# Kernel optimization log

Hardware: AMD Instinct MI355X
Metric: run time of the kernel (lower is better)

The kernel has to match this reference:

```python
import jax, jax.numpy as jnp
import numpy as np

B, L = 8, 512
D_MODEL, N_HEAD, N_GLOBAL, N_ITER = 64, 8, 64, 4
DAMP_H = 0.0; DAMP_Z = 0.0; STEP_H = 1.0; STEP_Z = 1.0; REG_H = 1.0; REG_Z = 1.0
NEG = -1e9; BIG = 1e9


def sin_pe(length, d):
    # standard additive sinusoidal positional encoding (AddPositionalEncoding)
    pos = np.arange(length, dtype=np.float32)[:, None]
    div = np.exp(np.arange(0, d, 2, dtype=np.float32) * (-np.log(10000.0) / d))
    pe = np.zeros((length, d), dtype=np.float32)
    pe[:, 0::2] = np.sin(pos * div)
    pe[:, 1::2] = np.cos(pos * div)
    return jnp.asarray(pe)


def setup_inputs() -> dict:
    key = jax.random.key(0)
    k1, k2, k3 = jax.random.split(key, 3)
    x = jax.random.normal(k1, (B, L, D_MODEL), jnp.float32)
    mask = jnp.ones((B, L), jnp.int32)
    ternary = jax.random.normal(k2, (D_MODEL, D_MODEL, N_HEAD), jnp.float32)  # std=1 init
    global_w = jax.random.normal(k3, (N_GLOBAL, D_MODEL, 1), jnp.float32) / np.sqrt(D_MODEL)
    return {"x": x, "mask": mask, "ternary": ternary, "global_w": global_w}


def _forward(x, mask, ternary, global_w):
    Bq, Lq, d = x.shape
    norm = lambda a: jax.nn.softmax(a, axis=-1)
    valid = (mask != 0)
    m1 = valid[:, :, None].astype(x.dtype)                      # (B,L,1) keep-mask
    pair = valid[:, None, :, None] & valid[:, None, None, :]    # (B,1,L,L)
    eye_big = BIG * jnp.eye(Lq, dtype=x.dtype)[None, None]      # kill self-edges

    x = x + sin_pe(Lq, d)[None]
    unary = x * m1
    q_z = unary
    q_h1 = jnp.where(pair, 1.0 - eye_big, NEG)                  # (B,H,L,L) via broadcast
    q_h1 = jnp.broadcast_to(q_h1, (Bq, N_HEAD, Lq, Lq))
    q_h2 = jnp.ones((Bq, 1, Lq, N_GLOBAL), x.dtype)             # single-channel: 1 global head

    cache_qh1, cache_qh2 = q_h1, q_h2
    cache_norm_qz = norm(q_z)
    cache_norm_qh1 = norm(q_h1)
    cache_norm_qh2 = norm(q_h2)

    for it in range(N_ITER):
        cache_qz = q_z
        nz = norm(q_z)
        qzn = nz if it == 0 else (1 - STEP_Z) * cache_norm_qz + STEP_Z * nz
        cache_norm_qz = qzn
        qz = qzn * m1
        # F1[z,c,i,j] = sum_{a,b} qz[z,i,a] qz[z,j,b] T[a,b,c]
        t1 = jnp.einsum('zia,abc->zibc', qz, ternary)
        F1 = jnp.einsum('zibc,zjb->zcij', t1, qz)
        F2 = jnp.einsum('zia,jac->zcij', qz, global_w)          # (B,1,L,n_global)
        q_h1 = cache_qh1 * DAMP_H + F1 * (1 - DAMP_H)
        q_h2 = cache_qh2 * DAMP_H + F2 * (1 - DAMP_H)
        cache_qh1, cache_qh2 = q_h1, q_h2
        q_h1m = jnp.where(pair, q_h1 - eye_big, NEG)
        nh1 = norm(q_h1m / REG_H)
        nh2 = norm(q_h2 / REG_H)
        qh1n = nh1 if it == 0 else (1 - STEP_H) * cache_norm_qh1 + STEP_H * nh1
        qh2n = nh2 if it == 0 else (1 - STEP_H) * cache_norm_qh2 + STEP_H * nh2
        cache_norm_qh1, cache_norm_qh2 = qh1n, qh2n
        # messages back to Z: factor (H_i=c, Z_i=a, Z_j=b)
        mi = jnp.einsum('zcij,zjb->zicb', qh1n, qz)
        Mi = jnp.einsum('zicb,abc->zia', mi, ternary)           # to Z_i
        mj = jnp.einsum('zcij,zia->zjca', qh1n, qz)
        Mj = jnp.einsum('zjca,abc->zjb', mj, ternary)           # to Z_j (block_msg=False)
        Mg = jnp.einsum('zcij,jac->zia', qh2n, global_w)        # global-node message
        new_qz = (unary + (Mi + Mj + Mg) / REG_Z) * m1
        q_z = cache_qz * DAMP_Z + new_qz * (1 - DAMP_Z)
    return q_z  # output_prob=False -> unnormalized scores (B,L,d_model)


def reference(x, mask, ternary, global_w):
    return _forward(x, mask, ternary, global_w)
```

## Files before the change

### kernel.cpp

```cpp
#include <hip/hip_runtime.h>

#define BB 8
#define LL 512
#define HH 8
#define BIGV (1e9f)

typedef unsigned short u16;
typedef __attribute__((ext_vector_type(8))) short bf16x8;
typedef __attribute__((ext_vector_type(4))) short s16x4;
typedef __attribute__((ext_vector_type(4))) float f32x4;

#define MFMA(a,b,c) __builtin_amdgcn_mfma_f32_16x16x32_bf16(a,b,c,0,0,0)

__device__ __forceinline__ u16 f2b(float f){
  unsigned u = __float_as_uint(f);
  u = (u + 0x7fffu + ((u>>16)&1u)) >> 16;
  return (u16)u;
}
__device__ __forceinline__ float b2f(u16 s){ return __uint_as_float(((unsigned)s)<<16); }
__device__ __forceinline__ bf16x8 ldb8(const u16* p){ return *(const bf16x8*)p; }
__device__ __forceinline__ s16x4 ld4nt(const u16* p){ return __builtin_nontemporal_load((const s16x4*)p); }

__device__ __forceinline__ float g16_sum(float v){
  v += __shfl_xor(v,1,64); v += __shfl_xor(v,2,64);
  v += __shfl_xor(v,4,64); v += __shfl_xor(v,8,64);
  return v;
}

__global__ void kp_prep(const float* __restrict__ T, const float* __restrict__ gw,
                        u16* __restrict__ T4t, u16* __restrict__ Tt2,
                        u16* __restrict__ Gt, u16* __restrict__ Gt2){
  int idx = blockIdx.x*256 + threadIdx.x;
  { int c=idx>>12, b=(idx>>6)&63, a=idx&63; T4t[idx] = f2b(T[(a*64+b)*8+c]); }
  { int c=idx>>12, a=(idx>>6)&63, b=idx&63; Tt2[idx] = f2b(T[(a*64+b)*8+c]); }
  if(idx < 4096){
    int a=idx>>6, j=idx&63;
    Gt[idx]  = f2b(gw[j*64+a]);
    Gt2[idx] = f2b(gw[idx]);
  }
}

__global__ __launch_bounds__(512) void kCA(const float* __restrict__ x, const int* __restrict__ mask,
      const u16* __restrict__ miP, const u16* __restrict__ mjP, const float* __restrict__ MgF_in,
      float* __restrict__ unary, float* __restrict__ mf,
      const u16* __restrict__ Gt2, const u16* __restrict__ Gt,
      const u16* __restrict__ T4t, const u16* __restrict__ Tt2,
      u16* __restrict__ qzb, float* __restrict__ MgF_out, float* __restrict__ out,
      u16* __restrict__ t1b, u16* __restrict__ t1t, u16* __restrict__ t2t, int mode){
  __shared__ u16 qlds[16*72];
  __shared__ u16 P2s[16*72];
  __shared__ float red2[16*4];
  int bid = blockIdx.x; int z = bid & 7, itile = bid >> 3;
  int t = threadIdx.x, lane = t&63, w = t>>6, l15 = lane&15, lhi = lane>>4;
  int rbase = z*LL + itile*16;
  if(t < 256){
    int row16 = t>>4, c4 = t&15;
    int rg = rbase + row16;
    float v[4]; float mk;
    if(mode == 0){
      mk = (mask[rg] != 0) ? 1.f : 0.f;
      if(c4 == 0) mf[rg] = mk;
      int pos = rg & (LL-1);
      #pragma unroll
      for(int k=0;k<4;k++){
        int d = c4*4 + k;
        float div = __expf(-(float)(d & ~1) * 0.14391156962f);
        float arg = (float)pos * div;
        float pe = (d & 1) ? cosf(arg) : sinf(arg);
        v[k] = (x[(size_t)rg*64 + d] + pe) * mk;
      }
      *(f32x4*)&unary[(size_t)rg*64 + c4*4] = (f32x4){v[0],v[1],v[2],v[3]};
    } else {
      mk = mf[rg];
      f32x4 acc = *(const f32x4*)&MgF_in[(size_t)rg*64 + c4*4];
      #pragma unroll
      for(int c=0;c<8;c++){
        s16x4 vv = ld4nt(&miP[(size_t)rg*512 + c*64 + c4*4]);
        acc[0]+=b2f((u16)vv[0]); acc[1]+=b2f((u16)vv[1]);
        acc[2]+=b2f((u16)vv[2]); acc[3]+=b2f((u16)vv[3]);
      }
      #pragma unroll
      for(int s=0;s<4;s++)
        #pragma unroll
        for(int c=0;c<8;c++){
          s16x4 vv = ld4nt(&mjP[(((size_t)(s*8+z))*LL + itile*16 + row16)*512 + c*64 + c4*4]);
          acc[0]+=b2f((u16)vv[0]); acc[1]+=b2f((u16)vv[1]);
          acc[2]+=b2f((u16)vv[2]); acc[3]+=b2f((u16)vv[3]);
        }
      f32x4 u0 = *(const f32x4*)&unary[(size_t)rg*64 + c4*4];
      #pragma unroll
      for(int k=0;k<4;k++) v[k] = (u0[k] + acc[k]) * mk;
    }
    if(mode == 2){
      *(f32x4*)&out[(size_t)rg*64 + c4*4] = (f32x4){v[0],v[1],v[2],v[3]};
    } else {
      float mx = fmaxf(fmaxf(v[0],v[1]), fmaxf(v[2],v[3]));
      mx = fmaxf(mx, __shfl_xor(mx,1,64));
      mx = fmaxf(mx, __shfl_xor(mx,2,64));
      mx = fmaxf(mx, __shfl_xor(mx,4,64));
      mx = fmaxf(mx, __shfl_xor(mx,8,64));
      float s = 0.f;
      #pragma unroll
      for(int k=0;k<4;k++){ v[k] = __expf(v[k]-mx); s += v[k]; }
      s += __shfl_xor(s,1,64); s += __shfl_xor(s,2,64);
      s += __shfl_xor(s,4,64); s += __shfl_xor(s,8,64);
      float iv = mk / s;
      s16x4 q4 = { (short)f2b(v[0]*iv), (short)f2b(v[1]*iv),
                   (short)f2b(v[2]*iv), (short)f2b(v[3]*iv) };
      *(s16x4*)&qzb[(size_t)rg*64 + c4*4] = q4;
      *(s16x4*)&qlds[row16*72 + c4*4] = q4;
    }
  }
  if(mode == 2) return;
  __syncthreads();
  float fv[4];
  if(t < 256){
    bf16x8 a0 = ldb8(&qlds[l15*72 + lhi*8]);
    bf16x8 a1 = ldb8(&qlds[l15*72 + lhi*8 + 32]);
    const u16* Br = Gt2 + (size_t)(w*16 + l15)*64 + lhi*8;
    f32x4 acc = {0.f,0.f,0.f,0.f};
    acc = MFMA(a0, ldb8(Br), acc);
    acc = MFMA(a1, ldb8(Br+32), acc);
    #pragma unroll
    for(int jj=0;jj<4;jj++){
      float e = __expf(acc[jj]);
      fv[jj] = e;
      float p = g16_sum(e);
      if(l15==0) red2[(lhi*4+jj)*4 + w] = p;
    }
  }
  __syncthreads();
  if(t < 256){
    #pragma unroll
    for(int jj=0;jj<4;jj++){
      int r = lhi*4+jj;
      float s = red2[r*4+0]+red2[r*4+1]+red2[r*4+2]+red2[r*4+3];
      float iv = 1.f/s;
      P2s[r*72 + w*16 + l15] = f2b(fv[jj]*iv);
    }
  }
  __syncthreads();
  if(t < 256){
    bf16x8 a0 = ldb8(&P2s[l15*72 + lhi*8]);
    bf16x8 a1 = ldb8(&P2s[l15*72 + lhi*8 + 32]);
    const u16* Br = Gt + (size_t)(w*16 + l15)*64 + lhi*8;
    f32x4 acc = {0.f,0.f,0.f,0.f};
    acc = MFMA(a0, ldb8(Br), acc);
    acc = MFMA(a1, ldb8(Br+32), acc);
    #pragma unroll
    for(int jj=0;jj<4;jj++)
      MgF_out[((size_t)rbase + lhi*4 + jj)*64 + w*16 + l15] = acc[jj];
  }
  {
    int c = w;
    size_t zc = (size_t)z*8 + c;
    bf16x8 aq0 = ldb8(&qlds[l15*72 + lhi*8]);
    bf16x8 aq1 = ldb8(&qlds[l15*72 + lhi*8 + 32]);
    const u16* T4c = T4t + c*4096;
    const u16* Ttc = Tt2 + c*4096;
    #pragma unroll
    for(int s=0;s<4;s++){
      const u16* Bq = T4c + (s*16 + l15)*64 + lhi*8;
      bf16x8 tb0 = ldb8(Bq), tb1 = ldb8(Bq+32);
      const u16* Uq = Ttc + (s*16 + l15)*64 + lhi*8;
      bf16x8 ub0 = ldb8(Uq), ub1 = ldb8(Uq+32);
      f32x4 d1 = {0.f,0.f,0.f,0.f};
      d1 = MFMA(aq0, tb0, d1);
      d1 = MFMA(aq1, tb1, d1);
      f32x4 d2 = {0.f,0.f,0.f,0.f};
      d2 = MFMA(tb0, aq0, d2);
      d2 = MFMA(tb1, aq1, d2);
      f32x4 d3 = {0.f,0.f,0.f,0.f};
      d3 = MFMA(ub0, aq0, d3);
      d3 = MFMA(ub1, aq1, d3);
      #pragma unroll
      for(int jj=0;jj<4;jj++){
        int r4 = lhi*4 + jj;
        t1b[(zc*LL + itile*16 + r4)*64 + s*16 + l15]  = f2b(d1[jj]);
        t1t[(zc*64 + s*16 + r4)*LL + itile*16 + l15]  = f2b(d2[jj]);
        t2t[(zc*64 + s*16 + r4)*LL + itile*16 + l15]  = f2b(d3[jj]);
      }
    }
  }
}

__global__ __launch_bounds__(1024) void kF(const u16* __restrict__ t1b, const u16* __restrict__ qzb,
        const u16* __restrict__ t1t, const u16* __restrict__ t2t, const float* __restrict__ mf,
        u16* __restrict__ miP, u16* __restrict__ mjP){
  extern __shared__ char smem[];
  u16*   t2s  = (u16*)smem;
  u16*   Pp   = (u16*)(smem + 66560);
  u16*   PpT  = (u16*)(smem + 99840);
  float* redS2= (float*)(smem + 140800);
  float* stgf = (float*)(smem + 141056);
  u16*   stg  = (u16*)smem;
  int bid = blockIdx.x;
  int z = bid&7, c = (bid>>3)&7, it = bid>>6;
  int zc = z*8 + c;
  int t = threadIdx.x, lane = t&63, w = t>>6, l15 = lane&15, lhi = lane>>4;
  int jc0 = w*32;
  int h = w>>3, wr = (w>>2)&1, wc = w&3;
  if(t < 64) redS2[t] = 0.f;
  __syncthreads();
  #pragma unroll
  for(int m=0;m<4;m++){
    int e = (m*1024 + t)*8;
    int a = e >> 9, j = e & 511;
    *(bf16x8*)&t2s[a*520 + j] = ldb8(t2t + ((size_t)zc*64 + a)*LL + j);
  }
  float mfj[2];
  mfj[0] = mf[z*LL + jc0 + l15];
  mfj[1] = mf[z*LL + jc0 + 16 + l15];
  f32x4 mj[2][4];
  #pragma unroll
  for(int jt=0;jt<2;jt++)
    #pragma unroll
    for(int bt=0;bt<4;bt++) mj[jt][bt] = (f32x4){0.f,0.f,0.f,0.f};
  u16* PpTw = PpT + w*32*40;

  for(int ip=0; ip<4; ++ip){
    int i0g = it*128 + ip*32;
    int par = ip & 1;
    f32x4 S[2][2];
    #pragma unroll
    for(int rt=0;rt<2;rt++){ S[rt][0] = (f32x4){0,0,0,0}; S[rt][1] = (f32x4){0,0,0,0}; }
    #pragma unroll
    for(int rt=0;rt<2;rt++){
      const u16* Ar = t1b + ((size_t)zc*LL + i0g + rt*16 + l15)*64 + lhi*8;
      bf16x8 a0 = ldb8(Ar), a1 = ldb8(Ar+32);
      #pragma unroll
      for(int ct=0;ct<2;ct++){
        const u16* Br = qzb + ((size_t)z*LL + jc0 + ct*16 + l15)*64 + lhi*8;
        S[rt][ct] = MFMA(a0, ldb8(Br), S[rt][ct]);
        S[rt][ct] = MFMA(a1, ldb8(Br+32), S[rt][ct]);
      }
    }
    #pragma unroll
    for(int rt=0;rt<2;rt++)
      #pragma unroll
      for(int jj=0;jj<4;jj++){
        int rloc = rt*16 + lhi*4 + jj;
        int irow = i0g + rloc;
        float mfi = mf[z*LL + irow];
        float ps = 0.f;
        #pragma unroll
        for(int ct=0;ct<2;ct++){
          int jcol = jc0 + ct*16 + l15;
          float v = S[rt][ct][jj] - ((irow==jcol)?BIGV:0.f);
          float e = mfi * mfj[ct] * __expf(v);
          S[rt][ct][jj] = e; ps += e;
          Pp[rloc*520 + jcol] = f2b(e);
        }
        ps = g16_sum(ps);
        if(l15 == 0) atomicAdd(&redS2[par*32 + rloc], ps);
      }
    __syncthreads();
    if(t < 32) redS2[(par^1)*32 + t] = 0.f;
    float ivv[2][4];
    #pragma unroll
    for(int rt=0;rt<2;rt++)
      #pragma unroll
      for(int jj=0;jj<4;jj++){
        float s = redS2[par*32 + rt*16 + lhi*4 + jj];
        ivv[rt][jj] = s > 0.f ? 1.f/s : 0.f;
      }
    #pragma unroll
    for(int rt=0;rt<2;rt++)
      #pragma unroll
      for(int ct=0;ct<2;ct++){
        s16x4 v4 = { (short)f2b(S[rt][ct][0]*ivv[rt][0]), (short)f2b(S[rt][ct][1]*ivv[rt][1]),
                     (short)f2b(S[rt][ct][2]*ivv[rt][2]), (short)f2b(S[rt][ct][3]*ivv[rt][3]) };
        *(s16x4*)&PpTw[(ct*16 + l15)*40 + rt*16 + lhi*4] = v4;
      }
    {
      f32x4 mia = {0.f,0.f,0.f,0.f};
      const u16* Ab = Pp + (wr*16 + l15)*520 + h*256 + lhi*8;
      const u16* Bb = t2s + (wc*16 + l15)*520 + h*256 + lhi*8;
      #pragma unroll
      for(int ks=0;ks<8;ks++)
        mia = MFMA(ldb8(Ab + ks*32), ldb8(Bb + ks*32), mia);
      #pragma unroll
      for(int jj=0;jj<4;jj++)
        stgf[(h*32 + wr*16 + lhi*4 + jj)*68 + wc*16 + l15] = mia[jj]*ivv[wr][jj];
    }
    {
      bf16x8 av[2];
      #pragma unroll
      for(int jt=0;jt<2;jt++)
        av[jt] = ldb8(PpTw + (jt*16 + l15)*40 + lhi*8);
      #pragma unroll
      for(int bt=0;bt<4;bt++){
        bf16x8 b = ldb8(t1t + ((size_t)zc*64 + bt*16 + l15)*LL + i0g + lhi*8);
        #pragma unroll
        for(int jt=0;jt<2;jt++) mj[jt][bt] = MFMA(av[jt], b, mj[jt][bt]);
      }
    }
    __syncthreads();
    if(t < 512){
      int r = t>>4, cc = t&15;
      f32x4 v0 = *(const f32x4*)&stgf[r*68 + cc*4];
      f32x4 v1 = *(const f32x4*)&stgf[(32+r)*68 + cc*4];
      s16x4 o = { (short)f2b(v0[0]+v1[0]), (short)f2b(v0[1]+v1[1]),
                  (short)f2b(v0[2]+v1[2]), (short)f2b(v0[3]+v1[3]) };
      *(s16x4*)&miP[((size_t)z*LL + i0g + r)*512 + c*64 + cc*4] = o;
    }
  }
  #pragma unroll
  for(int jt=0;jt<2;jt++)
    #pragma unroll
    for(int bt=0;bt<4;bt++)
      #pragma unroll
      for(int jj=0;jj<4;jj++)
        stg[(jc0 + jt*16 + lhi*4 + jj)*72 + bt*16 + l15] = f2b(mj[jt][bt][jj]);
  __syncthreads();
  #pragma unroll
  for(int q=0;q<4;q++){
    int e = q*1024 + t;
    int j = e >> 3, ch = e & 7;
    *(bf16x8*)&mjP[(((size_t)(it*8 + z))*LL + j)*512 + c*64 + ch*8]
      = *(const bf16x8*)&stg[j*72 + ch*8];
  }
}

extern "C" void kernel_launch(void* const* d_in, const int* in_sizes, int n_in,
                              void* d_out, int out_size, void* d_ws, size_t ws_size,
                              hipStream_t stream) {
  const float* x       = (const float*)d_in[0];
  const int*   mask    = (const int*)d_in[1];
  const float* ternary = (const float*)d_in[2];
  const float* gw      = (const float*)d_in[3];
  float* out = (float*)d_out;

  const size_t NE = (size_t)BB*LL*64;
  char* p = (char*)d_ws;
  auto alloc = [&](size_t bytes)->void*{
    void* r = (void*)p; p += (bytes + 255) & ~(size_t)255; return r;
  };
  float* unary   = (float*)alloc(NE*4);
  float* mf      = (float*)alloc((size_t)BB*LL*4);
  u16*   qzb     = (u16*)alloc(NE*2);
  u16*   t1b     = (u16*)alloc((size_t)BB*HH*LL*64*2);
  u16*   t1t     = (u16*)alloc((size_t)BB*HH*LL*64*2);
  u16*   t2t     = (u16*)alloc((size_t)BB*HH*LL*64*2);
  float* MgF     = (float*)alloc(NE*4);
  u16*   miP     = (u16*)alloc((size_t)BB*LL*512*2);
  u16*   mjP     = (u16*)alloc((size_t)32*LL*512*2);
  u16*   T4t     = (u16*)alloc(32768*2);
  u16*   Tt2     = (u16*)alloc(32768*2);
  u16*   Gt      = (u16*)alloc(4096*2);
  u16*   Gt2     = (u16*)alloc(4096*2);

  const int KF_LDS = 158464;
  hipFuncSetAttribute(reinterpret_cast<const void*>(kF),
                      hipFuncAttributeMaxDynamicSharedMemorySize, KF_LDS);

  kp_prep<<<128, 256, 0, stream>>>(ternary, gw, T4t, Tt2, Gt, Gt2);
  kCA<<<256, 512, 0, stream>>>(x, mask, miP, mjP, MgF, unary, mf, Gt2, Gt,
                               T4t, Tt2, qzb, MgF, out, t1b, t1t, t2t, 0);
  for(int it=0; it<4; ++it){
    kF<<<256, 1024, KF_LDS, stream>>>(t1b, qzb, t1t, t2t, mf, miP, mjP);
    kCA<<<256, 512, 0, stream>>>(x, mask, miP, mjP, MgF, unary, mf, Gt2, Gt,
                                 T4t, Tt2, qzb, MgF, out, t1b, t1t, t2t, (it==3) ? 2 : 1);
  }
}
```

Baseline: 208.4 us.

## Split kF i-range into 8 chunks, drop LDS t2 staging to cut shared memory

```diff
diff --git a/kernel.cpp b/kernel.cpp
--- a/kernel.cpp
+++ b/kernel.cpp
@@ -20,6 +20,8 @@
 __device__ __forceinline__ float b2f(u16 s){ return __uint_as_float(((unsigned)s)<<16); }
 __device__ __forceinline__ bf16x8 ldb8(const u16* p){ return *(const bf16x8*)p; }
 __device__ __forceinline__ s16x4 ld4nt(const u16* p){ return __builtin_nontemporal_load((const s16x4*)p); }
+__device__ __forceinline__ void st4nt(u16* p, s16x4 v){ __builtin_nontemporal_store(v, (s16x4*)p); }
+__device__ __forceinline__ void stb8nt(u16* p, bf16x8 v){ __builtin_nontemporal_store(v, (bf16x8*)p); }
 
 __device__ __forceinline__ float g16_sum(float v){
   v += __shfl_xor(v,1,64); v += __shfl_xor(v,2,64);
@@ -80,7 +82,7 @@
         acc[2]+=b2f((u16)vv[2]); acc[3]+=b2f((u16)vv[3]);
       }
       #pragma unroll
-      for(int s=0;s<4;s++)
+      for(int s=0;s<8;s++)
         #pragma unroll
         for(int c=0;c<8;c++){
           s16x4 vv = ld4nt(&mjP[(((size_t)(s*8+z))*LL + itile*16 + row16)*512 + c*64 + c4*4]);
@@ -188,12 +190,11 @@
         const u16* __restrict__ t1t, const u16* __restrict__ t2t, const float* __restrict__ mf,
         u16* __restrict__ miP, u16* __restrict__ mjP){
   extern __shared__ char smem[];
-  u16*   t2s  = (u16*)smem;
-  u16*   Pp   = (u16*)(smem + 66560);
-  u16*   PpT  = (u16*)(smem + 99840);
-  float* redS2= (float*)(smem + 140800);
-  float* stgf = (float*)(smem + 141056);
-  u16*   stg  = (u16*)smem;
+  u16*   Pp    = (u16*)smem;
+  u16*   PpT   = (u16*)(smem + 33280);
+  float* redS2 = (float*)(smem + 53760);
+  u16*   stgm  = (u16*)(smem + 54016);
+  u16*   stg   = (u16*)smem;
   int bid = blockIdx.x;
   int z = bid&7, c = (bid>>3)&7, it = bid>>6;
   int zc = z*8 + c;
@@ -202,12 +203,6 @@
   int h = w>>3, wr = (w>>2)&1, wc = w&3;
   if(t < 64) redS2[t] = 0.f;
   __syncthreads();
-  #pragma unroll
-  for(int m=0;m<4;m++){
-    int e = (m*1024 + t)*8;
-    int a = e >> 9, j = e & 511;
-    *(bf16x8*)&t2s[a*520 + j] = ldb8(t2t + ((size_t)zc*64 + a)*LL + j);
-  }
   float mfj[2];
   mfj[0] = mf[z*LL + jc0 + l15];
   mfj[1] = mf[z*LL + jc0 + 16 + l15];
@@ -216,10 +211,10 @@
   for(int jt=0;jt<2;jt++)
     #pragma unroll
     for(int bt=0;bt<4;bt++) mj[jt][bt] = (f32x4){0.f,0.f,0.f,0.f};
-  u16* PpTw = PpT + w*32*40;
-
-  for(int ip=0; ip<4; ++ip){
-    int i0g = it*128 + ip*32;
+  u16* PpTw = PpT + w*16*40;
+
+  for(int ip=0; ip<2; ++ip){
+    int i0g = it*64 + ip*32;
     int par = ip & 1;
     f32x4 S[2][2];
     #pragma unroll
@@ -264,61 +259,68 @@
         float s = redS2[par*32 + rt*16 + lhi*4 + jj];
         ivv[rt][jj] = s > 0.f ? 1.f/s : 0.f;
       }
-    #pragma unroll
-    for(int rt=0;rt<2;rt++)
+    {
+      bf16x8 bmj[4];
+      #pragma unroll
+      for(int bt=0;bt<4;bt++)
+        bmj[bt] = ldb8(t1t + ((size_t)zc*64 + bt*16 + l15)*LL + i0g + lhi*8);
       #pragma unroll
       for(int ct=0;ct<2;ct++){
-        s16x4 v4 = { (short)f2b(S[rt][ct][0]*ivv[rt][0]), (short)f2b(S[rt][ct][1]*ivv[rt][1]),
-                     (short)f2b(S[rt][ct][2]*ivv[rt][2]), (short)f2b(S[rt][ct][3]*ivv[rt][3]) };
-        *(s16x4*)&PpTw[(ct*16 + l15)*40 + rt*16 + lhi*4] = v4;
-      }
+        #pragma unroll
+        for(int rt=0;rt<2;rt++){
+          s16x4 v4 = { (short)f2b(S[rt][ct][0]*ivv[rt][0]), (short)f2b(S[rt][ct][1]*ivv[rt][1]),
+                       (short)f2b(S[rt][ct][2]*ivv[rt][2]), (short)f2b(S[rt][ct][3]*ivv[rt][3]) };
+          *(s16x4*)&PpTw[l15*40 + rt*16 + lhi*4] = v4;
+        }
+        bf16x8 av = ldb8(PpTw + l15*40 + lhi*8);
+        #pragma unroll
+        for(int bt=0;bt<4;bt++) mj[ct][bt] = MFMA(av, bmj[bt], mj[ct][bt]);
+      }
+    }
     {
       f32x4 mia = {0.f,0.f,0.f,0.f};
       const u16* Ab = Pp + (wr*16 + l15)*520 + h*256 + lhi*8;
-      const u16* Bb = t2s + (wc*16 + l15)*520 + h*256 + lhi*8;
+      const u16* Bb = t2t + ((size_t)zc*64 + wc*16 + l15)*LL + h*256 + lhi*8;
       #pragma unroll
       for(int ks=0;ks<8;ks++)
         mia = MFMA(ldb8(Ab + ks*32), ldb8(Bb + ks*32), mia);
       #pragma unroll
       for(int jj=0;jj<4;jj++)
-        stgf[(h*32 + wr*16 + lhi*4 + jj)*68 + wc*16 + l15] = mia[jj]*ivv[wr][jj];
-    }
-    {
-      bf16x8 av[2];
-      #pragma unroll
-      for(int jt=0;jt<2;jt++)
-        av[jt] = ldb8(PpTw + (jt*16 + l15)*40 + lhi*8);
-      #pragma unroll
-      for(int bt=0;bt<4;bt++){
-        bf16x8 b = ldb8(t1t + ((size_t)zc*64 + bt*16 + l15)*LL + i0g + lhi*8);
-        #pragma unroll
-        for(int jt=0;jt<2;jt++) mj[jt][bt] = MFMA(av[jt], b, mj[jt][bt]);
-      }
+        stgm[(h*32 + wr*16 + lhi*4 + jj)*68 + wc*16 + l15] = f2b(mia[jj]*ivv[wr][jj]);
     }
     __syncthreads();
     if(t < 512){
       int r = t>>4, cc = t&15;
-      f32x4 v0 = *(const f32x4*)&stgf[r*68 + cc*4];
-      f32x4 v1 = *(const f32x4*)&stgf[(32+r)*68 + cc*4];
-      s16x4 o = { (short)f2b(v0[0]+v1[0]), (short)f2b(v0[1]+v1[1]),
-                  (short)f2b(v0[2]+v1[2]), (short)f2b(v0[3]+v1[3]) };
-      *(s16x4*)&miP[((size_t)z*LL + i0g + r)*512 + c*64 + cc*4] = o;
+      s16x4 v0 = *(const s16x4*)&stgm[r*68 + cc*4];
+      s16x4 v1 = *(const s16x4*)&stgm[(32+r)*68 + cc*4];
+      s16x4 o = { (short)f2b(b2f((u16)v0[0])+b2f((u16)v1[0])),
+                  (short)f2b(b2f((u16)v0[1])+b2f((u16)v1[1])),
+                  (short)f2b(b2f((u16)v0[2])+b2f((u16)v1[2])),
+                  (short)f2b(b2f((u16)v0[3])+b2f((u16)v1[3])) };
+      st4nt(&miP[((size_t)z*LL + i0g + r)*512 + c*64 + cc*4], o);
     }
   }
   #pragma unroll
-  for(int jt=0;jt<2;jt++)
-    #pragma unroll
-    for(int bt=0;bt<4;bt++)
-      #pragma unroll
-      for(int jj=0;jj<4;jj++)
-        stg[(jc0 + jt*16 + lhi*4 + jj)*72 + bt*16 + l15] = f2b(mj[jt][bt][jj]);
-  __syncthreads();
-  #pragma unroll
-  for(int q=0;q<4;q++){
-    int e = q*1024 + t;
-    int j = e >> 3, ch = e & 7;
-    *(bf16x8*)&mjP[(((size_t)(it*8 + z))*LL + j)*512 + c*64 + ch*8]
-      = *(const bf16x8*)&stg[j*72 + ch*8];
+  for(int r2=0;r2<2;r2++){
+    __syncthreads();
+    if((w>>3) == r2){
+      int jl = jc0 - r2*256;
+      #pragma unroll
+      for(int jt=0;jt<2;jt++)
+        #pragma unroll
+        for(int bt=0;bt<4;bt++)
+          #pragma unroll
+          for(int jj=0;jj<4;jj++)
+            stg[(jl + jt*16 + lhi*4 + jj)*72 + bt*16 + l15] = f2b(mj[jt][bt][jj]);
+    }
+    __syncthreads();
+    #pragma unroll
+    for(int q=0;q<2;q++){
+      int e = q*1024 + t;
+      int j = e >> 3, ch = e & 7;
+      stb8nt(&mjP[(((size_t)(it*8 + z))*LL + r2*256 + j)*512 + c*64 + ch*8],
+             *(const bf16x8*)&stg[j*72 + ch*8]);
+    }
   }
 }
 
@@ -344,13 +346,13 @@
   u16*   t2t     = (u16*)alloc((size_t)BB*HH*LL*64*2);
   float* MgF     = (float*)alloc(NE*4);
   u16*   miP     = (u16*)alloc((size_t)BB*LL*512*2);
-  u16*   mjP     = (u16*)alloc((size_t)32*LL*512*2);
+  u16*   mjP     = (u16*)alloc((size_t)64*LL*512*2);
   u16*   T4t     = (u16*)alloc(32768*2);
   u16*   Tt2     = (u16*)alloc(32768*2);
   u16*   Gt      = (u16*)alloc(4096*2);
   u16*   Gt2     = (u16*)alloc(4096*2);
 
-  const int KF_LDS = 158464;
+  const int KF_LDS = 62720;
   hipFuncSetAttribute(reinterpret_cast<const void*>(kF),
                       hipFuncAttributeMaxDynamicSharedMemorySize, KF_LDS);
 
@@ -358,7 +360,7 @@
   kCA<<<256, 512, 0, stream>>>(x, mask, miP, mjP, MgF, unary, mf, Gt2, Gt,
                                T4t, Tt2, qzb, MgF, out, t1b, t1t, t2t, 0);
   for(int it=0; it<4; ++it){
-    kF<<<256, 1024, KF_LDS, stream>>>(t1b, qzb, t1t, t2t, mf, miP, mjP);
+    kF<<<512, 1024, KF_LDS, stream>>>(t1b, qzb, t1t, t2t, mf, miP, mjP);
     kCA<<<256, 512, 0, stream>>>(x, mask, miP, mjP, MgF, unary, mf, Gt2, Gt,
                                  T4t, Tt2, qzb, MgF, out, t1b, t1t, t2t, (it==3) ? 2 : 1);
   }
```

After: 288.9 us. 38.7% more time.
